# Kernel tuning notes

Hardware: AMD Instinct MI355X
Metric: run time of the kernel (lower is better)

Reference implementation:

```python
import jax, jax.numpy as jnp
import numpy as np

T, B, D, H = 512, 64, 256, 512


def setup_inputs() -> dict:
    key = jax.random.key(0)
    ks = jax.random.split(key, 6)
    scale = 1.0 / np.sqrt(D + H)
    return {
        "seqs": jax.random.normal(ks[0], (T, B, D), dtype=jnp.float32),
        "h": jnp.zeros((B, H), dtype=jnp.float32),
        "C": jnp.zeros((B, H), dtype=jnp.float32),
        "Wi": jax.random.normal(ks[1], (H, D + H), dtype=jnp.float32) * scale,
        "bi": jnp.zeros((H,), dtype=jnp.float32),
        "Wf": jax.random.normal(ks[2], (H, D + H), dtype=jnp.float32) * scale,
        "bf": jnp.zeros((H,), dtype=jnp.float32),
        "Wg": jax.random.normal(ks[3], (H, D + H), dtype=jnp.float32) * scale,
        "bg": jnp.zeros((H,), dtype=jnp.float32),
        "Wo": jax.random.normal(ks[4], (H, D + H), dtype=jnp.float32) * scale,
        "bo": jnp.zeros((H,), dtype=jnp.float32),
    }


def reference(seqs, h, C, Wi, bi, Wf, bf, Wg, bg, Wo, bo):
    # Fuse the 4 gate Linears into one matmul: W [4H, D+H], b [4H].
    W = jnp.concatenate([Wi, Wf, Wg, Wo], axis=0)
    b = jnp.concatenate([bi, bf, bg, bo], axis=0)

    def step(carry, x):
        h_t, c_t = carry
        merge = jnp.concatenate([h_t, x], axis=1)  # [B, H+D] (h first, as in torch code)
        gates = merge @ W.T + b                    # [B, 4H]
        i, f, g, o = jnp.split(gates, 4, axis=1)
        c_new = jax.nn.sigmoid(f) * c_t + jax.nn.sigmoid(i) * jnp.tanh(g)
        h_new = jax.nn.sigmoid(o) * jnp.tanh(c_new)
        return (h_new, c_new), h_new

    (_, cT), hs = jax.lax.scan(step, (h, C), seqs)
    allhidden = jnp.concatenate([h[None], hs], axis=0)  # [T+1, B, H], includes initial h
    return allhidden, cT
```

## Files before the change

### kernel.cpp

```cpp
#include <hip/hip_runtime.h>


#define TSTEPS 512
#define BATCH 64
#define DIN 256
#define HID 512
#define KTOT 768
#define BHID (BATCH * HID)
#define NB 8
#define NU 16
#define VROW 1064
#define POISON 0x7f7f7f7fu

typedef __attribute__((ext_vector_type(8))) short bf16x8;
typedef __attribute__((ext_vector_type(4))) float f32x4;

__device__ __forceinline__ float4 llc_load4(const float* p) {
    float4 r; asm volatile("global_load_dwordx4 %0, %1, off sc0 sc1" : "=&v"(r) : "v"(p)); return r;
}
__device__ __forceinline__ void llc_store1(float* p, float v) {
    asm volatile("global_store_dword %0, %1, off sc0 sc1" :: "v"(p), "v"(v) : "memory");
}
__device__ __forceinline__ unsigned short f2bf(float f) {
    unsigned u = __float_as_uint(f);
    return (unsigned short)((u + 0x7fffu + ((u >> 16) & 1u)) >> 16);
}

__global__ __launch_bounds__(256, 1)
void lstm_persistent(const float* __restrict__ seqs,
                     const float* __restrict__ h0,
                     const float* __restrict__ c0,
                     const float* __restrict__ Wi, const float* __restrict__ bi,
                     const float* __restrict__ Wf, const float* __restrict__ bff,
                     const float* __restrict__ Wg, const float* __restrict__ bg,
                     const float* __restrict__ Wo, const float* __restrict__ bo,
                     float* __restrict__ out)
{
    __shared__ __align__(16) short vv[NB * VROW];

    const int tid  = threadIdx.x;
    const int bid  = blockIdx.x;
    const int g    = bid >> 5;
    const int rblk = bid & 31;
    const int b0 = g * NB;
    const int u0 = rblk * NU;

    const int wv  = tid >> 6;
    const int l   = tid & 63;
    const int n16 = l & 15;
    const int khi = (l >> 4) & 3;
    const int bbr = l & 7;

    const int gsel = n16 & 3;
    const float* Wsel = (gsel == 0) ? Wi : (gsel == 1) ? Wf : (gsel == 2) ? Wg : Wo;
    const float* wrow = Wsel + (size_t)(u0 + 4 * wv + (n16 >> 2)) * KTOT;
    bf16x8 whi[24], wlo[24];
#pragma unroll
    for (int kt = 0; kt < 24; ++kt) {
        const int k0 = kt * 32 + khi * 8;
        const float4 a = *reinterpret_cast<const float4*>(wrow + k0);
        const float4 b = *reinterpret_cast<const float4*>(wrow + k0 + 4);
        const float vals[8] = {a.x, a.y, a.z, a.w, b.x, b.y, b.z, b.w};
        bf16x8 h8, l8;
#pragma unroll
        for (int i = 0; i < 8; ++i) {
            const unsigned short hv = f2bf(vals[i]);
            h8[i] = (short)hv;
            l8[i] = (short)f2bf(vals[i] - __uint_as_float((unsigned)hv << 16));
        }
        whi[kt] = h8; wlo[kt] = l8;
    }

    const int unit_d  = u0 + 4 * wv + khi;
    const int batch_d = b0 + (n16 & 7);
    const float bI = bi[unit_d],  bF = bff[unit_d];
    const float bG = bg[unit_d],  bO = bo[unit_d];
    float creg = c0[(size_t)batch_d * HID + unit_d];

    if (tid < 128) {
        const int uu = tid & 15, bb = tid >> 4;
        out[(size_t)(b0 + bb) * HID + u0 + uu] = h0[(size_t)(b0 + bb) * HID + u0 + uu];
    }

    {
        const int b = tid >> 5, k0 = (tid & 31) * 16;
        const float* hp = h0 + (size_t)(b0 + b) * HID + k0;
        float hv[16];
#pragma unroll
        for (int i = 0; i < 4; ++i) {
            const float4 t4 = reinterpret_cast<const float4*>(hp)[i];
            hv[4*i] = t4.x; hv[4*i+1] = t4.y; hv[4*i+2] = t4.z; hv[4*i+3] = t4.w;
        }
        bf16x8 a8, b8;
#pragma unroll
        for (int i = 0; i < 8; ++i) { a8[i] = (short)f2bf(hv[i]); b8[i] = (short)f2bf(hv[8+i]); }
        *reinterpret_cast<bf16x8*>(&vv[b * VROW + k0])     = a8;
        *reinterpret_cast<bf16x8*>(&vv[b * VROW + k0 + 8]) = b8;
    }
    if (tid < 128) {
        const int b = tid >> 4, kx = (tid & 15) * 16;
        const float* xp = seqs + (size_t)(b0 + b) * DIN + kx;
        float xv[16];
#pragma unroll
        for (int i = 0; i < 4; ++i) {
            const float4 t4 = reinterpret_cast<const float4*>(xp)[i];
            xv[4*i] = t4.x; xv[4*i+1] = t4.y; xv[4*i+2] = t4.z; xv[4*i+3] = t4.w;
        }
        bf16x8 a8, b8, la8, lb8;
#pragma unroll
        for (int i = 0; i < 8; ++i) {
            const unsigned short h1 = f2bf(xv[i]);
            a8[i] = (short)h1; la8[i] = (short)f2bf(xv[i] - __uint_as_float((unsigned)h1 << 16));
            const unsigned short h2 = f2bf(xv[8+i]);
            b8[i] = (short)h2; lb8[i] = (short)f2bf(xv[8+i] - __uint_as_float((unsigned)h2 << 16));
        }
        *reinterpret_cast<bf16x8*>(&vv[b * VROW + 512 + kx])     = a8;
        *reinterpret_cast<bf16x8*>(&vv[b * VROW + 512 + kx + 8]) = b8;
        *reinterpret_cast<bf16x8*>(&vv[b * VROW + 768 + kx])     = la8;
        *reinterpret_cast<bf16x8*>(&vv[b * VROW + 768 + kx + 8]) = lb8;
    }
    __syncthreads();

    const short* vrow = &vv[bbr * VROW + khi * 8];

    for (int t = 0; t < TSTEPS; ++t) {
        f32x4 aA = {0.f,0.f,0.f,0.f}, aB = {0.f,0.f,0.f,0.f}, aC = {0.f,0.f,0.f,0.f};
#pragma unroll
        for (int kt = 0; kt < 8; ++kt) {
            const bf16x8 bh = *reinterpret_cast<const bf16x8*>(vrow + 512 + kt * 32);
            const bf16x8 bl = *reinterpret_cast<const bf16x8*>(vrow + 768 + kt * 32);
            aA = __builtin_amdgcn_mfma_f32_16x16x32_bf16(whi[16 + kt], bh, aA, 0, 0, 0);
            aB = __builtin_amdgcn_mfma_f32_16x16x32_bf16(wlo[16 + kt], bh, aB, 0, 0, 0);
            aC = __builtin_amdgcn_mfma_f32_16x16x32_bf16(whi[16 + kt], bl, aC, 0, 0, 0);
        }

        float4 xr[4];
        const bool do_x = (t + 1 < TSTEPS) && (tid < 128);
        if (do_x) {
            const float* xp = seqs + (size_t)(t + 1) * BATCH * DIN
                            + (size_t)(b0 + (tid >> 4)) * DIN + (tid & 15) * 16;
#pragma unroll
            for (int i = 0; i < 4; ++i) xr[i] = reinterpret_cast<const float4*>(xp)[i];
        }

        if (t > 0) {
            const int b = tid >> 5, k0 = (tid & 31) * 16;
            const float* hp = out + (size_t)t * BHID + (size_t)(b0 + b) * HID + k0;
            float4 hb[4];
            unsigned miss = 0;
            for (;;) {
#pragma unroll
                for (int i = 0; i < 4; ++i) hb[i] = llc_load4(hp + 4 * i);
                asm volatile("s_waitcnt vmcnt(0)" ::: "memory");
                __builtin_amdgcn_sched_barrier(0);
                bool ok = true;
#pragma unroll
                for (int i = 0; i < 4; ++i) {
                    ok &= (__float_as_uint(hb[i].x) != POISON);
                    ok &= (__float_as_uint(hb[i].y) != POISON);
                    ok &= (__float_as_uint(hb[i].z) != POISON);
                    ok &= (__float_as_uint(hb[i].w) != POISON);
                }
                if (ok) break;
                if (++miss > (1u << 20)) break;
                __builtin_amdgcn_s_sleep(1);
            }
            float hv[16];
#pragma unroll
            for (int i = 0; i < 4; ++i) {
                hv[4*i] = hb[i].x; hv[4*i+1] = hb[i].y; hv[4*i+2] = hb[i].z; hv[4*i+3] = hb[i].w;
            }
            bf16x8 a8, b8;
#pragma unroll
            for (int i = 0; i < 8; ++i) { a8[i] = (short)f2bf(hv[i]); b8[i] = (short)f2bf(hv[8+i]); }
            *reinterpret_cast<bf16x8*>(&vv[b * VROW + k0])     = a8;
            *reinterpret_cast<bf16x8*>(&vv[b * VROW + k0 + 8]) = b8;
        }
        __syncthreads();

#pragma unroll
        for (int kt = 0; kt < 16; ++kt) {
            const bf16x8 bh = *reinterpret_cast<const bf16x8*>(vrow + kt * 32);
            aA = __builtin_amdgcn_mfma_f32_16x16x32_bf16(whi[kt], bh, aA, 0, 0, 0);
            aB = __builtin_amdgcn_mfma_f32_16x16x32_bf16(wlo[kt], bh, aB, 0, 0, 0);
        }
        const f32x4 gA = aA + aB + aC;

        if (n16 < 8) {
            const float gi = gA[0] + bI;
            const float gf = gA[1] + bF;
            const float gG = gA[2] + bG;
            const float go = gA[3] + bO;
            const float i_ = 1.f / (1.f + __expf(-gi));
            const float f_ = 1.f / (1.f + __expf(-gf));
            const float o_ = 1.f / (1.f + __expf(-go));
            float eg = __expf(-2.f * fabsf(gG));
            float tg = (1.f - eg) / (1.f + eg);
            tg = (gG < 0.f) ? -tg : tg;
            creg = f_ * creg + i_ * tg;
            float ec = __expf(-2.f * fabsf(creg));
            float tc = (1.f - ec) / (1.f + ec);
            tc = (creg < 0.f) ? -tc : tc;
            const float hn = o_ * tc;
            llc_store1(out + (size_t)(t + 1) * BHID + (size_t)batch_d * HID + unit_d, hn);
            if (t == TSTEPS - 1)
                out[(size_t)(TSTEPS + 1) * BHID + (size_t)batch_d * HID + unit_d] = creg;
        }

        if (do_x) {
            const int b = tid >> 4, kx = (tid & 15) * 16;
            float xv[16];
#pragma unroll
            for (int i = 0; i < 4; ++i) {
                xv[4*i] = xr[i].x; xv[4*i+1] = xr[i].y; xv[4*i+2] = xr[i].z; xv[4*i+3] = xr[i].w;
            }
            bf16x8 a8, b8, la8, lb8;
#pragma unroll
            for (int i = 0; i < 8; ++i) {
                const unsigned short h1 = f2bf(xv[i]);
                a8[i] = (short)h1; la8[i] = (short)f2bf(xv[i] - __uint_as_float((unsigned)h1 << 16));
                const unsigned short h2 = f2bf(xv[8+i]);
                b8[i] = (short)h2; lb8[i] = (short)f2bf(xv[8+i] - __uint_as_float((unsigned)h2 << 16));
            }
            *reinterpret_cast<bf16x8*>(&vv[b * VROW + 512 + kx])     = a8;
            *reinterpret_cast<bf16x8*>(&vv[b * VROW + 512 + kx + 8]) = b8;
            *reinterpret_cast<bf16x8*>(&vv[b * VROW + 768 + kx])     = la8;
            *reinterpret_cast<bf16x8*>(&vv[b * VROW + 768 + kx + 8]) = lb8;
        }
        __syncthreads();
    }
}

extern "C" void kernel_launch(void* const* d_in, const int* in_sizes, int n_in,
                              void* d_out, int out_size, void* d_ws, size_t ws_size,
                              hipStream_t stream) {
    const float* seqs = (const float*)d_in[0];
    const float* h0   = (const float*)d_in[1];
    const float* c0   = (const float*)d_in[2];
    const float* Wi   = (const float*)d_in[3];
    const float* bi   = (const float*)d_in[4];
    const float* Wf   = (const float*)d_in[5];
    const float* bf   = (const float*)d_in[6];
    const float* Wg   = (const float*)d_in[7];
    const float* bg   = (const float*)d_in[8];
    const float* Wo   = (const float*)d_in[9];
    const float* bo   = (const float*)d_in[10];
    float* out = (float*)d_out;

    hipMemsetAsync((char*)out + (size_t)BHID * 4, 0x7f,
                   (size_t)TSTEPS * BHID * 4, stream);

    hipLaunchKernelGGL(lstm_persistent, dim3(256), dim3(256), 0, stream,
                       seqs, h0, c0, Wi, bi, Wf, bf, Wg, bg, Wo, bo, out);
}
```

Measured before the change: 1.355 ms.

## Halve block count with 512-thread blocks covering 32 units each, prefetch h earlier

Each block now covers 32 hidden units with 8 waves instead of 16 units with 4 waves, so 128 blocks run instead of 256. This halves the number of blocks polling each step's h from the last-level cache, spreading the h and x staging loads across more threads. The llc loads of h are also issued at the top of the step, before the x-part MFMAs, so their latency overlaps compute. The cost is fewer CUs in use and larger blocks that must synchronise more waves each step.

New measurement: 1.251 ms (median of 2 runs). 7.7% less time.

```diff
diff --git a/kernel.cpp b/kernel.cpp
--- a/kernel.cpp
+++ b/kernel.cpp
@@ -8,7 +8,7 @@
 #define KTOT 768
 #define BHID (BATCH * HID)
 #define NB 8
-#define NU 16
+#define NU 32
 #define VROW 1064
 #define POISON 0x7f7f7f7fu
 
@@ -26,7 +26,7 @@
     return (unsigned short)((u + 0x7fffu + ((u >> 16) & 1u)) >> 16);
 }
 
-__global__ __launch_bounds__(256, 1)
+__global__ __launch_bounds__(512, 1)
 void lstm_persistent(const float* __restrict__ seqs,
                      const float* __restrict__ h0,
                      const float* __restrict__ c0,
@@ -40,8 +40,8 @@
 
     const int tid  = threadIdx.x;
     const int bid  = blockIdx.x;
-    const int g    = bid >> 5;
-    const int rblk = bid & 31;
+    const int g    = bid >> 4;
+    const int rblk = bid & 15;
     const int b0 = g * NB;
     const int u0 = rblk * NU;
 
@@ -77,53 +77,48 @@
     const float bG = bg[unit_d],  bO = bo[unit_d];
     float creg = c0[(size_t)batch_d * HID + unit_d];
 
-    if (tid < 128) {
-        const int uu = tid & 15, bb = tid >> 4;
+    if (tid < 256) {
+        const int uu = tid & 31, bb = tid >> 5;
         out[(size_t)(b0 + bb) * HID + u0 + uu] = h0[(size_t)(b0 + bb) * HID + u0 + uu];
     }
 
     {
-        const int b = tid >> 5, k0 = (tid & 31) * 16;
+        const int b = tid >> 6, k0 = (tid & 63) * 8;
         const float* hp = h0 + (size_t)(b0 + b) * HID + k0;
-        float hv[16];
-#pragma unroll
-        for (int i = 0; i < 4; ++i) {
-            const float4 t4 = reinterpret_cast<const float4*>(hp)[i];
-            hv[4*i] = t4.x; hv[4*i+1] = t4.y; hv[4*i+2] = t4.z; hv[4*i+3] = t4.w;
-        }
-        bf16x8 a8, b8;
-#pragma unroll
-        for (int i = 0; i < 8; ++i) { a8[i] = (short)f2bf(hv[i]); b8[i] = (short)f2bf(hv[8+i]); }
-        *reinterpret_cast<bf16x8*>(&vv[b * VROW + k0])     = a8;
-        *reinterpret_cast<bf16x8*>(&vv[b * VROW + k0 + 8]) = b8;
-    }
-    if (tid < 128) {
-        const int b = tid >> 4, kx = (tid & 15) * 16;
+        const float4 t0 = reinterpret_cast<const float4*>(hp)[0];
+        const float4 t1 = reinterpret_cast<const float4*>(hp)[1];
+        const float hv[8] = {t0.x, t0.y, t0.z, t0.w, t1.x, t1.y, t1.z, t1.w};
+        bf16x8 a8;
+#pragma unroll
+        for (int i = 0; i < 8; ++i) a8[i] = (short)f2bf(hv[i]);
+        *reinterpret_cast<bf16x8*>(&vv[b * VROW + k0]) = a8;
+    }
+    if (tid < 256) {
+        const int b = tid >> 5, kx = (tid & 31) * 8;
         const float* xp = seqs + (size_t)(b0 + b) * DIN + kx;
-        float xv[16];
-#pragma unroll
-        for (int i = 0; i < 4; ++i) {
-            const float4 t4 = reinterpret_cast<const float4*>(xp)[i];
-            xv[4*i] = t4.x; xv[4*i+1] = t4.y; xv[4*i+2] = t4.z; xv[4*i+3] = t4.w;
-        }
-        bf16x8 a8, b8, la8, lb8;
+        const float4 t0 = reinterpret_cast<const float4*>(xp)[0];
+        const float4 t1 = reinterpret_cast<const float4*>(xp)[1];
+        const float xv[8] = {t0.x, t0.y, t0.z, t0.w, t1.x, t1.y, t1.z, t1.w};
+        bf16x8 a8, la8;
 #pragma unroll
         for (int i = 0; i < 8; ++i) {
             const unsigned short h1 = f2bf(xv[i]);
-            a8[i] = (short)h1; la8[i] = (short)f2bf(xv[i] - __uint_as_float((unsigned)h1 << 16));
-            const unsigned short h2 = f2bf(xv[8+i]);
-            b8[i] = (short)h2; lb8[i] = (short)f2bf(xv[8+i] - __uint_as_float((unsigned)h2 << 16));
-        }
-        *reinterpret_cast<bf16x8*>(&vv[b * VROW + 512 + kx])     = a8;
-        *reinterpret_cast<bf16x8*>(&vv[b * VROW + 512 + kx + 8]) = b8;
-        *reinterpret_cast<bf16x8*>(&vv[b * VROW + 768 + kx])     = la8;
-        *reinterpret_cast<bf16x8*>(&vv[b * VROW + 768 + kx + 8]) = lb8;
+            a8[i]  = (short)h1;
+            la8[i] = (short)f2bf(xv[i] - __uint_as_float((unsigned)h1 << 16));
+        }
+        *reinterpret_cast<bf16x8*>(&vv[b * VROW + 512 + kx]) = a8;
+        *reinterpret_cast<bf16x8*>(&vv[b * VROW + 768 + kx]) = la8;
     }
     __syncthreads();
 
     const short* vrow = &vv[bbr * VROW + khi * 8];
 
     for (int t = 0; t < TSTEPS; ++t) {
+        const int cb = tid >> 6, ck = (tid & 63) * 8;
+        const float* hpf = out + (size_t)t * BHID + (size_t)(b0 + cb) * HID + ck;
+        float4 hb0, hb1;
+        if (t > 0) { hb0 = llc_load4(hpf); hb1 = llc_load4(hpf + 4); }
+
         f32x4 aA = {0.f,0.f,0.f,0.f}, aB = {0.f,0.f,0.f,0.f}, aC = {0.f,0.f,0.f,0.f};
 #pragma unroll
         for (int kt = 0; kt < 8; ++kt) {
@@ -134,47 +129,39 @@
             aC = __builtin_amdgcn_mfma_f32_16x16x32_bf16(whi[16 + kt], bl, aC, 0, 0, 0);
         }
 
-        float4 xr[4];
-        const bool do_x = (t + 1 < TSTEPS) && (tid < 128);
+        float4 xr0, xr1;
+        const bool do_x = (t + 1 < TSTEPS) && (tid < 256);
         if (do_x) {
             const float* xp = seqs + (size_t)(t + 1) * BATCH * DIN
-                            + (size_t)(b0 + (tid >> 4)) * DIN + (tid & 15) * 16;
-#pragma unroll
-            for (int i = 0; i < 4; ++i) xr[i] = reinterpret_cast<const float4*>(xp)[i];
+                            + (size_t)(b0 + (tid >> 5)) * DIN + (tid & 31) * 8;
+            xr0 = reinterpret_cast<const float4*>(xp)[0];
+            xr1 = reinterpret_cast<const float4*>(xp)[1];
         }
 
         if (t > 0) {
-            const int b = tid >> 5, k0 = (tid & 31) * 16;
-            const float* hp = out + (size_t)t * BHID + (size_t)(b0 + b) * HID + k0;
-            float4 hb[4];
             unsigned miss = 0;
             for (;;) {
-#pragma unroll
-                for (int i = 0; i < 4; ++i) hb[i] = llc_load4(hp + 4 * i);
                 asm volatile("s_waitcnt vmcnt(0)" ::: "memory");
                 __builtin_amdgcn_sched_barrier(0);
                 bool ok = true;
-#pragma unroll
-                for (int i = 0; i < 4; ++i) {
-                    ok &= (__float_as_uint(hb[i].x) != POISON);
-                    ok &= (__float_as_uint(hb[i].y) != POISON);
-                    ok &= (__float_as_uint(hb[i].z) != POISON);
-                    ok &= (__float_as_uint(hb[i].w) != POISON);
-                }
+                ok &= (__float_as_uint(hb0.x) != POISON);
+                ok &= (__float_as_uint(hb0.y) != POISON);
+                ok &= (__float_as_uint(hb0.z) != POISON);
+                ok &= (__float_as_uint(hb0.w) != POISON);
+                ok &= (__float_as_uint(hb1.x) != POISON);
+                ok &= (__float_as_uint(hb1.y) != POISON);
+                ok &= (__float_as_uint(hb1.z) != POISON);
+                ok &= (__float_as_uint(hb1.w) != POISON);
                 if (ok) break;
                 if (++miss > (1u << 20)) break;
                 __builtin_amdgcn_s_sleep(1);
+                hb0 = llc_load4(hpf); hb1 = llc_load4(hpf + 4);
             }
-            float hv[16];
-#pragma unroll
-            for (int i = 0; i < 4; ++i) {
-                hv[4*i] = hb[i].x; hv[4*i+1] = hb[i].y; hv[4*i+2] = hb[i].z; hv[4*i+3] = hb[i].w;
-            }
-            bf16x8 a8, b8;
-#pragma unroll
-            for (int i = 0; i < 8; ++i) { a8[i] = (short)f2bf(hv[i]); b8[i] = (short)f2bf(hv[8+i]); }
-            *reinterpret_cast<bf16x8*>(&vv[b * VROW + k0])     = a8;
-            *reinterpret_cast<bf16x8*>(&vv[b * VROW + k0 + 8]) = b8;
+            const float hv[8] = {hb0.x, hb0.y, hb0.z, hb0.w, hb1.x, hb1.y, hb1.z, hb1.w};
+            bf16x8 a8;
+#pragma unroll
+            for (int i = 0; i < 8; ++i) a8[i] = (short)f2bf(hv[i]);
+            *reinterpret_cast<bf16x8*>(&vv[cb * VROW + ck]) = a8;
         }
         __syncthreads();
 
@@ -208,24 +195,17 @@
         }
 
         if (do_x) {
-            const int b = tid >> 4, kx = (tid & 15) * 16;
-            float xv[16];
-#pragma unroll
-            for (int i = 0; i < 4; ++i) {
-                xv[4*i] = xr[i].x; xv[4*i+1] = xr[i].y; xv[4*i+2] = xr[i].z; xv[4*i+3] = xr[i].w;
-            }
-            bf16x8 a8, b8, la8, lb8;
+            const int b = tid >> 5, kx = (tid & 31) * 8;
+            const float xv[8] = {xr0.x, xr0.y, xr0.z, xr0.w, xr1.x, xr1.y, xr1.z, xr1.w};
+            bf16x8 a8, la8;
 #pragma unroll
             for (int i = 0; i < 8; ++i) {
                 const unsigned short h1 = f2bf(xv[i]);
-                a8[i] = (short)h1; la8[i] = (short)f2bf(xv[i] - __uint_as_float((unsigned)h1 << 16));
-                const unsigned short h2 = f2bf(xv[8+i]);
-                b8[i] = (short)h2; lb8[i] = (short)f2bf(xv[8+i] - __uint_as_float((unsigned)h2 << 16));
+                a8[i]  = (short)h1;
+                la8[i] = (short)f2bf(xv[i] - __uint_as_float((unsigned)h1 << 16));
             }
-            *reinterpret_cast<bf16x8*>(&vv[b * VROW + 512 + kx])     = a8;
-            *reinterpret_cast<bf16x8*>(&vv[b * VROW + 512 + kx + 8]) = b8;
-            *reinterpret_cast<bf16x8*>(&vv[b * VROW + 768 + kx])     = la8;
-            *reinterpret_cast<bf16x8*>(&vv[b * VROW + 768 + kx + 8]) = lb8;
+            *reinterpret_cast<bf16x8*>(&vv[b * VROW + 512 + kx]) = a8;
+            *reinterpret_cast<bf16x8*>(&vv[b * VROW + 768 + kx]) = la8;
         }
         __syncthreads();
     }
@@ -250,6 +230,6 @@
     hipMemsetAsync((char*)out + (size_t)BHID * 4, 0x7f,
                    (size_t)TSTEPS * BHID * 4, stream);
 
-    hipLaunchKernelGGL(lstm_persistent, dim3(256), dim3(256), 0, stream,
+    hipLaunchKernelGGL(lstm_persistent, dim3(128), dim3(512), 0, stream,
                        seqs, h0, c0, Wi, bi, Wf, bf, Wg, bg, Wo, bo, out);
 }
```
